# Optimization experiments

Measured on AMD Instinct MI355X. Metric: run time of the kernel, lower is better.

## Reference

```python
import jax, jax.numpy as jnp
import numpy as np

H1 = 51  # lstm1 hidden size
H2 = 1   # lstm2 hidden size


def _lstm_cell(x, h, c, Wih, Whh, bih, bhh):
    # PyTorch LSTMCell: gates = x W_ih^T + b_ih + h W_hh^T + b_hh, order i,f,g,o
    gates = x @ Wih.T + h @ Whh.T + (bih + bhh)
    i, f, g, o = jnp.split(gates, 4, axis=-1)
    i = jax.nn.sigmoid(i)
    f = jax.nn.sigmoid(f)
    g = jnp.tanh(g)
    o = jax.nn.sigmoid(o)
    c_new = f * c + i * g
    h_new = o * jnp.tanh(c_new)
    return h_new, c_new


def setup_inputs() -> dict:
    key = jax.random.key(0)
    ks = jax.random.split(key, 9)
    B, T = 2048, 1024
    s1 = 1.0 / np.sqrt(H1)
    s2 = 1.0 / np.sqrt(H2)
    u = lambda k, shape, s: jax.random.uniform(k, shape, jnp.float32, -s, s)
    return {
        "input": jax.random.normal(ks[0], (B, T), dtype=jnp.float32),
        "W_ih1": u(ks[1], (4 * H1, 1), s1),
        "W_hh1": u(ks[2], (4 * H1, H1), s1),
        "b_ih1": u(ks[3], (4 * H1,), s1),
        "b_hh1": u(ks[4], (4 * H1,), s1),
        "W_ih2": u(ks[5], (4 * H2, H1), s2),
        "W_hh2": u(ks[6], (4 * H2, H2), s2),
        "b_ih2": u(ks[7], (4 * H2,), s2),
        "b_hh2": u(ks[8], (4 * H2,), s2),
        "future": 64,
    }


def reference(input, W_ih1, W_hh1, b_ih1, b_hh1, W_ih2, W_hh2, b_ih2, b_hh2, future):
    B = input.shape[0]
    dt = input.dtype
    h1 = jnp.zeros((B, H1), dt)
    c1 = jnp.zeros((B, H1), dt)
    h2 = jnp.zeros((B, H2), dt)
    c2 = jnp.zeros((B, H2), dt)

    def step(carry, x_t):
        h1, c1, h2, c2 = carry
        h1, c1 = _lstm_cell(x_t, h1, c1, W_ih1, W_hh1, b_ih1, b_hh1)
        h2, c2 = _lstm_cell(h1, h2, c2, W_ih2, W_hh2, b_ih2, b_hh2)
        return (h1, c1, h2, c2), h2

    xs = jnp.swapaxes(input, 0, 1)[:, :, None]  # [T, B, 1]
    carry, outs = jax.lax.scan(step, (h1, c1, h2, c2), xs)

    def step_future(carry, _):
        h1, c1, h2, c2 = carry
        h1, c1 = _lstm_cell(h2, h1, c1, W_ih1, W_hh1, b_ih1, b_hh1)
        h2, c2 = _lstm_cell(h1, h2, c2, W_ih2, W_hh2, b_ih2, b_hh2)
        return (h1, c1, h2, c2), h2

    if future > 0:
        _, outs_f = jax.lax.scan(step_future, carry, None, length=future)
        outs = jnp.concatenate([outs, outs_f], axis=0)

    # [T+F, B, 1] -> [B, T+F]
    return jnp.swapaxes(outs[:, :, 0], 0, 1)
```

## Files before the change

kernel.cpp:

```cpp
#include <hip/hip_runtime.h>


#define H1N 51
#define NP  26
#define WAVE 64

typedef float v2f __attribute__((ext_vector_type(2)));

#define INV_LN2  1.44269504088896340736f
#define INV_LN2X2 2.88539008177792681472f

__device__ __forceinline__ float sigmoid_s(float xs) {
    return __builtin_amdgcn_rcpf(1.0f + __builtin_amdgcn_exp2f(-xs));
}
__device__ __forceinline__ float tanh_s2(float xs2) {
    float e = __builtin_amdgcn_exp2f(xs2);
    return fmaf(-2.0f, __builtin_amdgcn_rcpf(e + 1.0f), 1.0f);
}
__device__ __forceinline__ float tanh_nat(float x) {
    return tanh_s2(x * INV_LN2X2);
}
__device__ __forceinline__ float rdlane(float v, int k) {
    return __int_as_float(__builtin_amdgcn_readlane(__float_as_int(v), k));
}

template<int CTRL, int RM, int BM>
__device__ __forceinline__ void dpp_stage4(float& a, float& b, float& c, float& d) {
    int ta = __builtin_amdgcn_update_dpp(0, __float_as_int(a), CTRL, RM, BM, false);
    int tb = __builtin_amdgcn_update_dpp(0, __float_as_int(b), CTRL, RM, BM, false);
    int tc = __builtin_amdgcn_update_dpp(0, __float_as_int(c), CTRL, RM, BM, false);
    int td = __builtin_amdgcn_update_dpp(0, __float_as_int(d), CTRL, RM, BM, false);
    a += __int_as_float(ta); b += __int_as_float(tb);
    c += __int_as_float(tc); d += __int_as_float(td);
}

__global__ __attribute__((amdgpu_flat_work_group_size(64, 64),
                          amdgpu_waves_per_eu(2, 2)))
void lstm_seq(const float* __restrict__ input,
              const float* __restrict__ W_ih1,
              const float* __restrict__ W_hh1,
              const float* __restrict__ b_ih1,
              const float* __restrict__ b_hh1,
              const float* __restrict__ W_ih2,
              const float* __restrict__ W_hh2,
              const float* __restrict__ b_ih2,
              const float* __restrict__ b_hh2,
              float* __restrict__ out,
              int T, int TF)
{
    const int j   = threadIdx.x;
    const bool jv = (j < H1N);
    const int jj  = jv ? j : 0;
    const float m = jv ? 1.0f : 0.0f;
    const int b   = blockIdx.x;

    const int r_i = jj, r_f = H1N + jj, r_g = 2*H1N + jj, r_o = 3*H1N + jj;

    const float s_i = m * INV_LN2, s_f = m * INV_LN2;
    const float s_g = m * INV_LN2X2, s_o = m * INV_LN2;

    v2f wI[NP], wF[NP], wG[NP], wO[NP];
#pragma unroll
    for (int kk = 0; kk < NP; ++kk) {
        const int k0 = 2*kk, k1 = 2*kk + 1;
        const float n0 = (k0 < H1N) ? 1.0f : 0.0f;
        const float n1 = (k1 < H1N) ? 1.0f : 0.0f;
        const int c0 = (k0 < H1N) ? k0 : 0, c1i = (k1 < H1N) ? k1 : 0;
        wI[kk].x = s_i * n0 * W_hh1[r_i*H1N + c0];  wI[kk].y = s_i * n1 * W_hh1[r_i*H1N + c1i];
        wF[kk].x = s_f * n0 * W_hh1[r_f*H1N + c0];  wF[kk].y = s_f * n1 * W_hh1[r_f*H1N + c1i];
        wG[kk].x = s_g * n0 * W_hh1[r_g*H1N + c0];  wG[kk].y = s_g * n1 * W_hh1[r_g*H1N + c1i];
        wO[kk].x = s_o * n0 * W_hh1[r_o*H1N + c0];  wO[kk].y = s_o * n1 * W_hh1[r_o*H1N + c1i];
    }
    const float b_i = s_i * (b_ih1[r_i] + b_hh1[r_i]);
    const float b_f = s_f * (b_ih1[r_f] + b_hh1[r_f]);
    const float b_g = s_g * (b_ih1[r_g] + b_hh1[r_g]);
    const float b_o = s_o * (b_ih1[r_o] + b_hh1[r_o]);
    const float wx_i = s_i * W_ih1[r_i];
    const float wx_f = s_f * W_ih1[r_f];
    const float wx_g = s_g * W_ih1[r_g];
    const float wx_o = s_o * W_ih1[r_o];

    float wi2_0 = m * INV_LN2   * W_ih2[0*H1N + jj];
    float wi2_1 = m * INV_LN2   * W_ih2[1*H1N + jj];
    float wi2_2 = m * INV_LN2X2 * W_ih2[2*H1N + jj];
    float wi2_3 = m * INV_LN2   * W_ih2[3*H1N + jj];
    const float wh2_0 = INV_LN2*W_hh2[0], wh2_1 = INV_LN2*W_hh2[1];
    const float wh2_2 = INV_LN2X2*W_hh2[2], wh2_3 = INV_LN2*W_hh2[3];
    const float b2_0 = INV_LN2*(b_ih2[0] + b_hh2[0]), b2_1 = INV_LN2*(b_ih2[1] + b_hh2[1]);
    const float b2_2 = INV_LN2X2*(b_ih2[2] + b_hh2[2]), b2_3 = INV_LN2*(b_ih2[3] + b_hh2[3]);

    float h1 = 0.0f, c1 = 0.0f, h2 = 0.0f, c2 = 0.0f;

    const float* __restrict__ xrow = input + (long)b * T;
    float*       __restrict__ orow = out   + (long)b * TF;

    float xbuf = 0.0f;
    float obuf = 0.0f;

    for (int t = 0; t < TF; ++t) {
        asm volatile("" : "+v"(wi2_0), "+v"(wi2_1), "+v"(wi2_2), "+v"(wi2_3));

        float x;
        if (t < T) {
            if ((t & 63) == 0) xbuf = xrow[t + j];
            x = rdlane(xbuf, t & 63);
        } else {
            x = h2;
        }

        v2f aI = {fmaf(wx_i, x, b_i), 0.0f};
        v2f aF = {fmaf(wx_f, x, b_f), 0.0f};
        v2f aG = {fmaf(wx_g, x, b_g), 0.0f};
        v2f aO = {fmaf(wx_o, x, b_o), 0.0f};
#pragma unroll
        for (int kk = 0; kk < NP; ++kk) {
            const unsigned int hlo =
                (unsigned int)__builtin_amdgcn_readlane(__float_as_int(h1), 2*kk);
            const unsigned int hhi =
                (unsigned int)__builtin_amdgcn_readlane(__float_as_int(h1), 2*kk + 1);
            const unsigned long long hp =
                ((unsigned long long)hhi << 32) | (unsigned long long)hlo;
            asm("v_pk_fma_f32 %0, %4, %8, %0\n\t"
                "v_pk_fma_f32 %1, %5, %8, %1\n\t"
                "v_pk_fma_f32 %2, %6, %8, %2\n\t"
                "v_pk_fma_f32 %3, %7, %8, %3"
                : "+v"(aI), "+v"(aF), "+v"(aG), "+v"(aO),
                  "+v"(wI[kk]), "+v"(wF[kk]), "+v"(wG[kk]), "+v"(wO[kk])
                : "s"(hp));
        }
        const float gi = sigmoid_s(aI.x + aI.y);
        const float gf = sigmoid_s(aF.x + aF.y);
        const float gg = tanh_s2 (aG.x + aG.y);
        const float go = sigmoid_s(aO.x + aO.y);
        c1 = fmaf(gf, c1, gi * gg);
        h1 = go * tanh_nat(c1);

        float p0 = wi2_0 * h1, p1 = wi2_1 * h1, p2 = wi2_2 * h1, p3 = wi2_3 * h1;
        dpp_stage4<0x111, 0xf, 0xf>(p0, p1, p2, p3);
        dpp_stage4<0x112, 0xf, 0xf>(p0, p1, p2, p3);
        dpp_stage4<0x114, 0xf, 0xe>(p0, p1, p2, p3);
        dpp_stage4<0x118, 0xf, 0xc>(p0, p1, p2, p3);
        dpp_stage4<0x142, 0xa, 0xf>(p0, p1, p2, p3);
        dpp_stage4<0x143, 0xc, 0xf>(p0, p1, p2, p3);
        p0 = rdlane(p0, 63); p1 = rdlane(p1, 63);
        p2 = rdlane(p2, 63); p3 = rdlane(p3, 63);

        const float g2i = sigmoid_s(fmaf(wh2_0, h2, b2_0 + p0));
        const float g2f = sigmoid_s(fmaf(wh2_1, h2, b2_1 + p1));
        const float g2g = tanh_s2 (fmaf(wh2_2, h2, b2_2 + p2));
        const float g2o = sigmoid_s(fmaf(wh2_3, h2, b2_3 + p3));
        c2 = fmaf(g2f, c2, g2i * g2g);
        h2 = g2o * tanh_nat(c2);

        if (j == (t & 63)) obuf = h2;
        if ((t & 63) == 63) orow[t - 63 + j] = obuf;
    }
}

extern "C" void kernel_launch(void* const* d_in, const int* in_sizes, int n_in,
                              void* d_out, int out_size, void* d_ws, size_t ws_size,
                              hipStream_t stream) {
    const float* input = (const float*)d_in[0];
    const float* W_ih1 = (const float*)d_in[1];
    const float* W_hh1 = (const float*)d_in[2];
    const float* b_ih1 = (const float*)d_in[3];
    const float* b_hh1 = (const float*)d_in[4];
    const float* W_ih2 = (const float*)d_in[5];
    const float* W_hh2 = (const float*)d_in[6];
    const float* b_ih2 = (const float*)d_in[7];
    const float* b_hh2 = (const float*)d_in[8];
    float* out = (float*)d_out;

    const int B  = 2048;
    const int T  = in_sizes[0] / B;
    const int TF = out_size   / B;

    lstm_seq<<<dim3(B), dim3(WAVE), 0, stream>>>(
        input, W_ih1, W_hh1, b_ih1, b_hh1, W_ih2, W_hh2, b_ih2, b_hh2,
        out, T, TF);
}
```

Baseline: 1.321 ms.

## Split LSTM into layer-1 pass, batched layer-2 pass, and future pass

During the teacher-forced phase the layer-2 cell does not feed back into layer 1, so the single fused kernel is split in three. The first kernel runs the layer-1 recurrence and writes the four reduced layer-2 input projections per step to workspace. A second kernel, one thread per batch row, runs the scalar layer-2 recurrence, and a third handles the autoregressive future steps. Layer 1 now reads h1 from LDS instead of readlane broadcasts, which takes the serial layer-2 chain off the layer-1 critical path, at the cost of about 32MB of extra workspace traffic and two more launches.

New measurement: 1.505 ms. 1.14x slower.

```diff
diff --git a/kernel.cpp b/kernel.cpp
--- a/kernel.cpp
+++ b/kernel.cpp
@@ -4,10 +4,11 @@
 #define H1N 51
 #define NP  26
 #define WAVE 64
+#define BATCH 2048
 
 typedef float v2f __attribute__((ext_vector_type(2)));
 
-#define INV_LN2  1.44269504088896340736f
+#define INV_LN2   1.44269504088896340736f
 #define INV_LN2X2 2.88539008177792681472f
 
 __device__ __forceinline__ float sigmoid_s(float xs) {
@@ -33,20 +34,27 @@
     a += __int_as_float(ta); b += __int_as_float(tb);
     c += __int_as_float(tc); d += __int_as_float(td);
 }
+__device__ __forceinline__ void wave_sum4(float& p0, float& p1, float& p2, float& p3) {
+    dpp_stage4<0x111, 0xf, 0xf>(p0, p1, p2, p3);
+    dpp_stage4<0x112, 0xf, 0xf>(p0, p1, p2, p3);
+    dpp_stage4<0x114, 0xf, 0xe>(p0, p1, p2, p3);
+    dpp_stage4<0x118, 0xf, 0xc>(p0, p1, p2, p3);
+    dpp_stage4<0x142, 0xa, 0xf>(p0, p1, p2, p3);
+    dpp_stage4<0x143, 0xc, 0xf>(p0, p1, p2, p3);
+}
 
 __global__ __attribute__((amdgpu_flat_work_group_size(64, 64),
                           amdgpu_waves_per_eu(2, 2)))
-void lstm_seq(const float* __restrict__ input,
-              const float* __restrict__ W_ih1,
-              const float* __restrict__ W_hh1,
-              const float* __restrict__ b_ih1,
-              const float* __restrict__ b_hh1,
-              const float* __restrict__ W_ih2,
-              const float* __restrict__ W_hh2,
-              const float* __restrict__ b_ih2,
-              const float* __restrict__ b_hh2,
-              float* __restrict__ out,
-              int T, int TF)
+void lstm1_pass(const float* __restrict__ input,
+                const float* __restrict__ W_ih1,
+                const float* __restrict__ W_hh1,
+                const float* __restrict__ b_ih1,
+                const float* __restrict__ b_hh1,
+                const float* __restrict__ W_ih2,
+                float4* __restrict__ zws,
+                float* __restrict__ h1s,
+                float* __restrict__ c1s,
+                int T)
 {
     const int j   = threadIdx.x;
     const bool jv = (j < H1N);
@@ -55,7 +63,6 @@
     const int b   = blockIdx.x;
 
     const int r_i = jj, r_f = H1N + jj, r_g = 2*H1N + jj, r_o = 3*H1N + jj;
-
     const float s_i = m * INV_LN2, s_f = m * INV_LN2;
     const float s_g = m * INV_LN2X2, s_o = m * INV_LN2;
 
@@ -84,29 +91,142 @@
     float wi2_1 = m * INV_LN2   * W_ih2[1*H1N + jj];
     float wi2_2 = m * INV_LN2X2 * W_ih2[2*H1N + jj];
     float wi2_3 = m * INV_LN2   * W_ih2[3*H1N + jj];
+
+    __shared__ __align__(16) float hrow[64];
+    hrow[j] = 0.0f;
+
+    float h1 = 0.0f, c1 = 0.0f;
+    const float* __restrict__ xrow = input + (long)b * T;
+    float xbuf = 0.0f;
+
+    for (int t = 0; t < T; ++t) {
+        asm volatile("" : "+v"(wi2_0), "+v"(wi2_1), "+v"(wi2_2), "+v"(wi2_3));
+
+        if ((t & 63) == 0) xbuf = xrow[t + j];
+        const float x = rdlane(xbuf, t & 63);
+
+        v2f aI = {fmaf(wx_i, x, b_i), 0.0f};
+        v2f aF = {fmaf(wx_f, x, b_f), 0.0f};
+        v2f aG = {fmaf(wx_g, x, b_g), 0.0f};
+        v2f aO = {fmaf(wx_o, x, b_o), 0.0f};
+#pragma unroll
+        for (int kk = 0; kk < NP; ++kk) {
+            const v2f hp = *(const v2f*)&hrow[2*kk];
+            asm("v_pk_fma_f32 %0, %4, %8, %0\n\t"
+                "v_pk_fma_f32 %1, %5, %8, %1\n\t"
+                "v_pk_fma_f32 %2, %6, %8, %2\n\t"
+                "v_pk_fma_f32 %3, %7, %8, %3"
+                : "+v"(aI), "+v"(aF), "+v"(aG), "+v"(aO),
+                  "+v"(wI[kk]), "+v"(wF[kk]), "+v"(wG[kk]), "+v"(wO[kk])
+                : "v"(hp));
+        }
+        const float gi = sigmoid_s(aI.x + aI.y);
+        const float gf = sigmoid_s(aF.x + aF.y);
+        const float gg = tanh_s2 (aG.x + aG.y);
+        const float go = sigmoid_s(aO.x + aO.y);
+        c1 = fmaf(gf, c1, gi * gg);
+        h1 = go * tanh_nat(c1);
+
+        hrow[j] = jv ? h1 : 0.0f;
+
+        float p0 = wi2_0 * h1, p1 = wi2_1 * h1, p2 = wi2_2 * h1, p3 = wi2_3 * h1;
+        wave_sum4(p0, p1, p2, p3);
+        if (j == 63) zws[(long)t * BATCH + b] = make_float4(p0, p1, p2, p3);
+    }
+
+    if (jv) { h1s[b*H1N + j] = h1; c1s[b*H1N + j] = c1; }
+}
+
+__global__ void lstm2_pass(const float4* __restrict__ zws,
+                           const float* __restrict__ W_hh2,
+                           const float* __restrict__ b_ih2,
+                           const float* __restrict__ b_hh2,
+                           float* __restrict__ out,
+                           float2* __restrict__ h2c2,
+                           int T, int TF)
+{
+    const int s = blockIdx.x * WAVE + threadIdx.x;
     const float wh2_0 = INV_LN2*W_hh2[0], wh2_1 = INV_LN2*W_hh2[1];
     const float wh2_2 = INV_LN2X2*W_hh2[2], wh2_3 = INV_LN2*W_hh2[3];
     const float b2_0 = INV_LN2*(b_ih2[0] + b_hh2[0]), b2_1 = INV_LN2*(b_ih2[1] + b_hh2[1]);
     const float b2_2 = INV_LN2X2*(b_ih2[2] + b_hh2[2]), b2_3 = INV_LN2*(b_ih2[3] + b_hh2[3]);
 
-    float h1 = 0.0f, c1 = 0.0f, h2 = 0.0f, c2 = 0.0f;
-
-    const float* __restrict__ xrow = input + (long)b * T;
-    float*       __restrict__ orow = out   + (long)b * TF;
-
-    float xbuf = 0.0f;
+    float h2 = 0.0f, c2 = 0.0f;
+    float* __restrict__ orow = out + (long)s * TF;
+    for (int t = 0; t < T; ++t) {
+        const float4 z = zws[(long)t * BATCH + s];
+        const float g2i = sigmoid_s(fmaf(wh2_0, h2, b2_0 + z.x));
+        const float g2f = sigmoid_s(fmaf(wh2_1, h2, b2_1 + z.y));
+        const float g2g = tanh_s2 (fmaf(wh2_2, h2, b2_2 + z.z));
+        const float g2o = sigmoid_s(fmaf(wh2_3, h2, b2_3 + z.w));
+        c2 = fmaf(g2f, c2, g2i * g2g);
+        h2 = g2o * tanh_nat(c2);
+        orow[t] = h2;
+    }
+    h2c2[s] = make_float2(h2, c2);
+}
+
+__global__ __attribute__((amdgpu_flat_work_group_size(64, 64),
+                          amdgpu_waves_per_eu(2, 2)))
+void lstm_future(const float* __restrict__ W_ih1, const float* __restrict__ W_hh1,
+                 const float* __restrict__ b_ih1, const float* __restrict__ b_hh1,
+                 const float* __restrict__ W_ih2, const float* __restrict__ W_hh2,
+                 const float* __restrict__ b_ih2, const float* __restrict__ b_hh2,
+                 const float* __restrict__ h1s, const float* __restrict__ c1s,
+                 const float2* __restrict__ h2c2,
+                 float* __restrict__ out, int T, int TF)
+{
+    const int j   = threadIdx.x;
+    const bool jv = (j < H1N);
+    const int jj  = jv ? j : 0;
+    const float m = jv ? 1.0f : 0.0f;
+    const int b   = blockIdx.x;
+
+    const int r_i = jj, r_f = H1N + jj, r_g = 2*H1N + jj, r_o = 3*H1N + jj;
+    const float s_i = m * INV_LN2, s_f = m * INV_LN2;
+    const float s_g = m * INV_LN2X2, s_o = m * INV_LN2;
+
+    v2f wI[NP], wF[NP], wG[NP], wO[NP];
+#pragma unroll
+    for (int kk = 0; kk < NP; ++kk) {
+        const int k0 = 2*kk, k1 = 2*kk + 1;
+        const float n0 = (k0 < H1N) ? 1.0f : 0.0f;
+        const float n1 = (k1 < H1N) ? 1.0f : 0.0f;
+        const int c0 = (k0 < H1N) ? k0 : 0, c1i = (k1 < H1N) ? k1 : 0;
+        wI[kk].x = s_i * n0 * W_hh1[r_i*H1N + c0];  wI[kk].y = s_i * n1 * W_hh1[r_i*H1N + c1i];
+        wF[kk].x = s_f * n0 * W_hh1[r_f*H1N + c0];  wF[kk].y = s_f * n1 * W_hh1[r_f*H1N + c1i];
+        wG[kk].x = s_g * n0 * W_hh1[r_g*H1N + c0];  wG[kk].y = s_g * n1 * W_hh1[r_g*H1N + c1i];
+        wO[kk].x = s_o * n0 * W_hh1[r_o*H1N + c0];  wO[kk].y = s_o * n1 * W_hh1[r_o*H1N + c1i];
+    }
+    const float b_i = s_i * (b_ih1[r_i] + b_hh1[r_i]);
+    const float b_f = s_f * (b_ih1[r_f] + b_hh1[r_f]);
+    const float b_g = s_g * (b_ih1[r_g] + b_hh1[r_g]);
+    const float b_o = s_o * (b_ih1[r_o] + b_hh1[r_o]);
+    const float wx_i = s_i * W_ih1[r_i];
+    const float wx_f = s_f * W_ih1[r_f];
+    const float wx_g = s_g * W_ih1[r_g];
+    const float wx_o = s_o * W_ih1[r_o];
+
+    float wi2_0 = m * INV_LN2   * W_ih2[0*H1N + jj];
+    float wi2_1 = m * INV_LN2   * W_ih2[1*H1N + jj];
+    float wi2_2 = m * INV_LN2X2 * W_ih2[2*H1N + jj];
+    float wi2_3 = m * INV_LN2   * W_ih2[3*H1N + jj];
+    const float wh2_0 = INV_LN2*W_hh2[0], wh2_1 = INV_LN2*W_hh2[1];
+    const float wh2_2 = INV_LN2X2*W_hh2[2], wh2_3 = INV_LN2*W_hh2[3];
+    const float b2_0 = INV_LN2*(b_ih2[0] + b_hh2[0]), b2_1 = INV_LN2*(b_ih2[1] + b_hh2[1]);
+    const float b2_2 = INV_LN2X2*(b_ih2[2] + b_hh2[2]), b2_3 = INV_LN2*(b_ih2[3] + b_hh2[3]);
+
+    float h1 = jv ? h1s[b*H1N + jj] : 0.0f;
+    float c1 = jv ? c1s[b*H1N + jj] : 0.0f;
+    const float2 st = h2c2[b];
+    float h2 = st.x, c2 = st.y;
+
+    float* __restrict__ orow = out + (long)b * TF;
     float obuf = 0.0f;
 
-    for (int t = 0; t < TF; ++t) {
+    for (int t = T; t < TF; ++t) {
         asm volatile("" : "+v"(wi2_0), "+v"(wi2_1), "+v"(wi2_2), "+v"(wi2_3));
-
-        float x;
-        if (t < T) {
-            if ((t & 63) == 0) xbuf = xrow[t + j];
-            x = rdlane(xbuf, t & 63);
-        } else {
-            x = h2;
-        }
+        const float x = h2;
 
         v2f aI = {fmaf(wx_i, x, b_i), 0.0f};
         v2f aF = {fmaf(wx_f, x, b_f), 0.0f};
@@ -136,12 +256,7 @@
         h1 = go * tanh_nat(c1);
 
         float p0 = wi2_0 * h1, p1 = wi2_1 * h1, p2 = wi2_2 * h1, p3 = wi2_3 * h1;
-        dpp_stage4<0x111, 0xf, 0xf>(p0, p1, p2, p3);
-        dpp_stage4<0x112, 0xf, 0xf>(p0, p1, p2, p3);
-        dpp_stage4<0x114, 0xf, 0xe>(p0, p1, p2, p3);
-        dpp_stage4<0x118, 0xf, 0xc>(p0, p1, p2, p3);
-        dpp_stage4<0x142, 0xa, 0xf>(p0, p1, p2, p3);
-        dpp_stage4<0x143, 0xc, 0xf>(p0, p1, p2, p3);
+        wave_sum4(p0, p1, p2, p3);
         p0 = rdlane(p0, 63); p1 = rdlane(p1, 63);
         p2 = rdlane(p2, 63); p3 = rdlane(p3, 63);
 
@@ -171,11 +286,22 @@
     const float* b_hh2 = (const float*)d_in[8];
     float* out = (float*)d_out;
 
-    const int B  = 2048;
+    const int B  = BATCH;
     const int T  = in_sizes[0] / B;
     const int TF = out_size   / B;
 
-    lstm_seq<<<dim3(B), dim3(WAVE), 0, stream>>>(
-        input, W_ih1, W_hh1, b_ih1, b_hh1, W_ih2, W_hh2, b_ih2, b_hh2,
-        out, T, TF);
-}
+    char* ws = (char*)d_ws;
+    float4* zws = (float4*)ws;
+    size_t off = (size_t)T * B * sizeof(float4);
+    float* h1s = (float*)(ws + off);  off += (size_t)B * H1N * sizeof(float);
+    float* c1s = (float*)(ws + off);  off += (size_t)B * H1N * sizeof(float);
+    float2* h2c2 = (float2*)(ws + off);
+
+    lstm1_pass<<<dim3(B), dim3(WAVE), 0, stream>>>(
+        input, W_ih1, W_hh1, b_ih1, b_hh1, W_ih2, zws, h1s, c1s, T);
+    lstm2_pass<<<dim3(B / WAVE), dim3(WAVE), 0, stream>>>(
+        zws, W_hh2, b_ih2, b_hh2, out, h2c2, T, TF);
+    lstm_future<<<dim3(B), dim3(WAVE), 0, stream>>>(
+        W_ih1, W_hh1, b_ih1, b_hh1, W_ih2, W_hh2, b_ih2, b_hh2,
+        h1s, c1s, h2c2, out, T, TF);
+}
```

## Process two sequences per wave and fold layer-2 projection into layer-1 matvec

Applied to the files above, without the earlier changes.

Each wave now handles two batch rows, sharing the register-resident W_hh1 weights across both recurrent matvecs. The hidden state is broadcast through LDS vector loads instead of per-element readlanes. The layer-2 input projection is folded into spare lanes 51-54 of the layer-1 matvec, with the bias packed into the padding column, which removes the DPP reduction. Layer 2 is skewed by one step, and occupancy drops to one wave per EU. The aim is less per-step latency per sequence, in exchange for fewer waves, more registers, and LDS round trips with no explicit barriers inside a single-wave block.

After: 1.290 ms. 2.3% less time.

```diff
diff --git a/kernel.cpp b/kernel.cpp
--- a/kernel.cpp
+++ b/kernel.cpp
@@ -1,13 +1,13 @@
 #include <hip/hip_runtime.h>
 
 
-#define H1N 51
-#define NP  26
+#define H1N  51
+#define NP   26
 #define WAVE 64
 
 typedef float v2f __attribute__((ext_vector_type(2)));
 
-#define INV_LN2  1.44269504088896340736f
+#define INV_LN2   1.44269504088896340736f
 #define INV_LN2X2 2.88539008177792681472f
 
 __device__ __forceinline__ float sigmoid_s(float xs) {
@@ -24,136 +24,162 @@
     return __int_as_float(__builtin_amdgcn_readlane(__float_as_int(v), k));
 }
 
-template<int CTRL, int RM, int BM>
-__device__ __forceinline__ void dpp_stage4(float& a, float& b, float& c, float& d) {
-    int ta = __builtin_amdgcn_update_dpp(0, __float_as_int(a), CTRL, RM, BM, false);
-    int tb = __builtin_amdgcn_update_dpp(0, __float_as_int(b), CTRL, RM, BM, false);
-    int tc = __builtin_amdgcn_update_dpp(0, __float_as_int(c), CTRL, RM, BM, false);
-    int td = __builtin_amdgcn_update_dpp(0, __float_as_int(d), CTRL, RM, BM, false);
-    a += __int_as_float(ta); b += __int_as_float(tb);
-    c += __int_as_float(tc); d += __int_as_float(td);
-}
-
 __global__ __attribute__((amdgpu_flat_work_group_size(64, 64),
-                          amdgpu_waves_per_eu(2, 2)))
-void lstm_seq(const float* __restrict__ input,
-              const float* __restrict__ W_ih1,
-              const float* __restrict__ W_hh1,
-              const float* __restrict__ b_ih1,
-              const float* __restrict__ b_hh1,
-              const float* __restrict__ W_ih2,
-              const float* __restrict__ W_hh2,
-              const float* __restrict__ b_ih2,
-              const float* __restrict__ b_hh2,
-              float* __restrict__ out,
-              int T, int TF)
+                          amdgpu_waves_per_eu(1, 1)))
+void lstm_seq2(const float* __restrict__ input,
+               const float* __restrict__ W_ih1,
+               const float* __restrict__ W_hh1,
+               const float* __restrict__ b_ih1,
+               const float* __restrict__ b_hh1,
+               const float* __restrict__ W_ih2,
+               const float* __restrict__ W_hh2,
+               const float* __restrict__ b_ih2,
+               const float* __restrict__ b_hh2,
+               float* __restrict__ out,
+               int T, int TF)
 {
     const int j   = threadIdx.x;
     const bool jv = (j < H1N);
     const int jj  = jv ? j : 0;
     const float m = jv ? 1.0f : 0.0f;
-    const int b   = blockIdx.x;
+    const bool isz = (j >= H1N) && (j < H1N + 4);
+    const int  q   = isz ? (j - H1N) : 0;
+    const float mz = isz ? 1.0f : 0.0f;
+    const float s2q = (q == 2) ? INV_LN2X2 : INV_LN2;
+
+    const int sA = 2 * blockIdx.x, sB = sA + 1;
 
     const int r_i = jj, r_f = H1N + jj, r_g = 2*H1N + jj, r_o = 3*H1N + jj;
-
-    const float s_i = m * INV_LN2, s_f = m * INV_LN2;
-    const float s_g = m * INV_LN2X2, s_o = m * INV_LN2;
+    const float s_i = INV_LN2, s_f = INV_LN2, s_g = INV_LN2X2, s_o = INV_LN2;
 
     v2f wI[NP], wF[NP], wG[NP], wO[NP];
 #pragma unroll
     for (int kk = 0; kk < NP; ++kk) {
-        const int k0 = 2*kk, k1 = 2*kk + 1;
-        const float n0 = (k0 < H1N) ? 1.0f : 0.0f;
-        const float n1 = (k1 < H1N) ? 1.0f : 0.0f;
-        const int c0 = (k0 < H1N) ? k0 : 0, c1i = (k1 < H1N) ? k1 : 0;
-        wI[kk].x = s_i * n0 * W_hh1[r_i*H1N + c0];  wI[kk].y = s_i * n1 * W_hh1[r_i*H1N + c1i];
-        wF[kk].x = s_f * n0 * W_hh1[r_f*H1N + c0];  wF[kk].y = s_f * n1 * W_hh1[r_f*H1N + c1i];
-        wG[kk].x = s_g * n0 * W_hh1[r_g*H1N + c0];  wG[kk].y = s_g * n1 * W_hh1[r_g*H1N + c1i];
-        wO[kk].x = s_o * n0 * W_hh1[r_o*H1N + c0];  wO[kk].y = s_o * n1 * W_hh1[r_o*H1N + c1i];
+        const int k0 = 2*kk, k1 = k0 + 1;
+        wI[kk].x = m*s_i*W_hh1[r_i*H1N + k0] + mz*s2q*W_ih2[q*H1N + k0];
+        wF[kk].x = m*s_f*W_hh1[r_f*H1N + k0];
+        wG[kk].x = m*s_g*W_hh1[r_g*H1N + k0];
+        wO[kk].x = m*s_o*W_hh1[r_o*H1N + k0];
+        if (k1 < H1N) {
+            wI[kk].y = m*s_i*W_hh1[r_i*H1N + k1] + mz*s2q*W_ih2[q*H1N + k1];
+            wF[kk].y = m*s_f*W_hh1[r_f*H1N + k1];
+            wG[kk].y = m*s_g*W_hh1[r_g*H1N + k1];
+            wO[kk].y = m*s_o*W_hh1[r_o*H1N + k1];
+        } else {
+            wI[kk].y = m*s_i*(b_ih1[r_i] + b_hh1[r_i]);
+            wF[kk].y = m*s_f*(b_ih1[r_f] + b_hh1[r_f]);
+            wG[kk].y = m*s_g*(b_ih1[r_g] + b_hh1[r_g]);
+            wO[kk].y = m*s_o*(b_ih1[r_o] + b_hh1[r_o]);
+        }
     }
-    const float b_i = s_i * (b_ih1[r_i] + b_hh1[r_i]);
-    const float b_f = s_f * (b_ih1[r_f] + b_hh1[r_f]);
-    const float b_g = s_g * (b_ih1[r_g] + b_hh1[r_g]);
-    const float b_o = s_o * (b_ih1[r_o] + b_hh1[r_o]);
-    const float wx_i = s_i * W_ih1[r_i];
-    const float wx_f = s_f * W_ih1[r_f];
-    const float wx_g = s_g * W_ih1[r_g];
-    const float wx_o = s_o * W_ih1[r_o];
-
-    float wi2_0 = m * INV_LN2   * W_ih2[0*H1N + jj];
-    float wi2_1 = m * INV_LN2   * W_ih2[1*H1N + jj];
-    float wi2_2 = m * INV_LN2X2 * W_ih2[2*H1N + jj];
-    float wi2_3 = m * INV_LN2   * W_ih2[3*H1N + jj];
+    const float wx_i = m*s_i*W_ih1[r_i];
+    const float wx_f = m*s_f*W_ih1[r_f];
+    const float wx_g = m*s_g*W_ih1[r_g];
+    const float wx_o = m*s_o*W_ih1[r_o];
+
     const float wh2_0 = INV_LN2*W_hh2[0], wh2_1 = INV_LN2*W_hh2[1];
     const float wh2_2 = INV_LN2X2*W_hh2[2], wh2_3 = INV_LN2*W_hh2[3];
     const float b2_0 = INV_LN2*(b_ih2[0] + b_hh2[0]), b2_1 = INV_LN2*(b_ih2[1] + b_hh2[1]);
     const float b2_2 = INV_LN2X2*(b_ih2[2] + b_hh2[2]), b2_3 = INV_LN2*(b_ih2[3] + b_hh2[3]);
 
-    float h1 = 0.0f, c1 = 0.0f, h2 = 0.0f, c2 = 0.0f;
-
-    const float* __restrict__ xrow = input + (long)b * T;
-    float*       __restrict__ orow = out   + (long)b * TF;
-
-    float xbuf = 0.0f;
-    float obuf = 0.0f;
-
-    for (int t = 0; t < TF; ++t) {
-        asm volatile("" : "+v"(wi2_0), "+v"(wi2_1), "+v"(wi2_2), "+v"(wi2_3));
-
-        float x;
-        if (t < T) {
-            if ((t & 63) == 0) xbuf = xrow[t + j];
-            x = rdlane(xbuf, t & 63);
-        } else {
-            x = h2;
-        }
-
-        v2f aI = {fmaf(wx_i, x, b_i), 0.0f};
-        v2f aF = {fmaf(wx_f, x, b_f), 0.0f};
-        v2f aG = {fmaf(wx_g, x, b_g), 0.0f};
-        v2f aO = {fmaf(wx_o, x, b_o), 0.0f};
+    __shared__ __align__(16) float hrowA[WAVE];
+    __shared__ __align__(16) float hrowB[WAVE];
+    __shared__ __align__(16) float2 zbuf[4];
+    hrowA[j] = (j == H1N) ? 1.0f : 0.0f;
+    hrowB[j] = (j == H1N) ? 1.0f : 0.0f;
+
+    float h1A = 0.0f, c1A = 0.0f, h2A = 0.0f, c2A = 0.0f;
+    float h1B = 0.0f, c1B = 0.0f, h2B = 0.0f, c2B = 0.0f;
+
+    const float* __restrict__ xrowA = input + (long)sA * T;
+    const float* __restrict__ xrowB = input + (long)sB * T;
+    float* __restrict__ orowA = out + (long)sA * TF;
+    float* __restrict__ orowB = out + (long)sB * TF;
+
+    float xbufA = 0.0f, xbufB = 0.0f, obufA = 0.0f, obufB = 0.0f;
+
+    for (int n = 0; n <= TF; ++n) {
+        v2f aIA = {0.0f, 0.0f}, aFA = {0.0f, 0.0f};
+        v2f aGA = {0.0f, 0.0f}, aOA = {0.0f, 0.0f};
+        v2f aIB = {0.0f, 0.0f}, aFB = {0.0f, 0.0f};
+        v2f aGB = {0.0f, 0.0f}, aOB = {0.0f, 0.0f};
 #pragma unroll
         for (int kk = 0; kk < NP; ++kk) {
-            const unsigned int hlo =
-                (unsigned int)__builtin_amdgcn_readlane(__float_as_int(h1), 2*kk);
-            const unsigned int hhi =
-                (unsigned int)__builtin_amdgcn_readlane(__float_as_int(h1), 2*kk + 1);
-            const unsigned long long hp =
-                ((unsigned long long)hhi << 32) | (unsigned long long)hlo;
-            asm("v_pk_fma_f32 %0, %4, %8, %0\n\t"
-                "v_pk_fma_f32 %1, %5, %8, %1\n\t"
-                "v_pk_fma_f32 %2, %6, %8, %2\n\t"
-                "v_pk_fma_f32 %3, %7, %8, %3"
-                : "+v"(aI), "+v"(aF), "+v"(aG), "+v"(aO),
+            const v2f hpA = *(const v2f*)&hrowA[2*kk];
+            const v2f hpB = *(const v2f*)&hrowB[2*kk];
+            asm("v_pk_fma_f32 %0, %8,  %12, %0\n\t"
+                "v_pk_fma_f32 %4, %8,  %13, %4\n\t"
+                "v_pk_fma_f32 %1, %9,  %12, %1\n\t"
+                "v_pk_fma_f32 %5, %9,  %13, %5\n\t"
+                "v_pk_fma_f32 %2, %10, %12, %2\n\t"
+                "v_pk_fma_f32 %6, %10, %13, %6\n\t"
+                "v_pk_fma_f32 %3, %11, %12, %3\n\t"
+                "v_pk_fma_f32 %7, %11, %13, %7"
+                : "+v"(aIA), "+v"(aFA), "+v"(aGA), "+v"(aOA),
+                  "+v"(aIB), "+v"(aFB), "+v"(aGB), "+v"(aOB),
                   "+v"(wI[kk]), "+v"(wF[kk]), "+v"(wG[kk]), "+v"(wO[kk])
-                : "s"(hp));
-        }
-        const float gi = sigmoid_s(aI.x + aI.y);
-        const float gf = sigmoid_s(aF.x + aF.y);
-        const float gg = tanh_s2 (aG.x + aG.y);
-        const float go = sigmoid_s(aO.x + aO.y);
-        c1 = fmaf(gf, c1, gi * gg);
-        h1 = go * tanh_nat(c1);
-
-        float p0 = wi2_0 * h1, p1 = wi2_1 * h1, p2 = wi2_2 * h1, p3 = wi2_3 * h1;
-        dpp_stage4<0x111, 0xf, 0xf>(p0, p1, p2, p3);
-        dpp_stage4<0x112, 0xf, 0xf>(p0, p1, p2, p3);
-        dpp_stage4<0x114, 0xf, 0xe>(p0, p1, p2, p3);
-        dpp_stage4<0x118, 0xf, 0xc>(p0, p1, p2, p3);
-        dpp_stage4<0x142, 0xa, 0xf>(p0, p1, p2, p3);
-        dpp_stage4<0x143, 0xc, 0xf>(p0, p1, p2, p3);
-        p0 = rdlane(p0, 63); p1 = rdlane(p1, 63);
-        p2 = rdlane(p2, 63); p3 = rdlane(p3, 63);
-
-        const float g2i = sigmoid_s(fmaf(wh2_0, h2, b2_0 + p0));
-        const float g2f = sigmoid_s(fmaf(wh2_1, h2, b2_1 + p1));
-        const float g2g = tanh_s2 (fmaf(wh2_2, h2, b2_2 + p2));
-        const float g2o = sigmoid_s(fmaf(wh2_3, h2, b2_3 + p3));
-        c2 = fmaf(g2f, c2, g2i * g2g);
-        h2 = g2o * tanh_nat(c2);
-
-        if (j == (t & 63)) obuf = h2;
-        if ((t & 63) == 63) orow[t - 63 + j] = obuf;
+                : "v"(hpA), "v"(hpB));
+        }
+        const float mIA = aIA.x + aIA.y, mIB = aIB.x + aIB.y;
+        if (isz) zbuf[q] = make_float2(mIA, mIB);
+        const float mFA = aFA.x + aFA.y, mFB = aFB.x + aFB.y;
+        const float mGA = aGA.x + aGA.y, mGB = aGB.x + aGB.y;
+        const float mOA = aOA.x + aOA.y, mOB = aOB.x + aOB.y;
+
+        if (n > 0) {
+            const float2 z0 = zbuf[0], z1 = zbuf[1], z2 = zbuf[2], z3 = zbuf[3];
+            {
+                const float g2i = sigmoid_s(fmaf(wh2_0, h2A, b2_0 + z0.x));
+                const float g2f = sigmoid_s(fmaf(wh2_1, h2A, b2_1 + z1.x));
+                const float g2g = tanh_s2 (fmaf(wh2_2, h2A, b2_2 + z2.x));
+                const float g2o = sigmoid_s(fmaf(wh2_3, h2A, b2_3 + z3.x));
+                c2A = fmaf(g2f, c2A, g2i * g2g);
+                h2A = g2o * tanh_nat(c2A);
+            }
+            {
+                const float g2i = sigmoid_s(fmaf(wh2_0, h2B, b2_0 + z0.y));
+                const float g2f = sigmoid_s(fmaf(wh2_1, h2B, b2_1 + z1.y));
+                const float g2g = tanh_s2 (fmaf(wh2_2, h2B, b2_2 + z2.y));
+                const float g2o = sigmoid_s(fmaf(wh2_3, h2B, b2_3 + z3.y));
+                c2B = fmaf(g2f, c2B, g2i * g2g);
+                h2B = g2o * tanh_nat(c2B);
+            }
+            const int tt = n - 1;
+            if (j == (tt & 63)) { obufA = h2A; obufB = h2B; }
+            if ((tt & 63) == 63) {
+                orowA[tt - 63 + j] = obufA;
+                orowB[tt - 63 + j] = obufB;
+            }
+        }
+
+        if (n < TF) {
+            float xA, xB;
+            if (n < T) {
+                if ((n & 63) == 0) { xbufA = xrowA[n + j]; xbufB = xrowB[n + j]; }
+                xA = rdlane(xbufA, n & 63);
+                xB = rdlane(xbufB, n & 63);
+            } else {
+                xA = h2A;
+                xB = h2B;
+            }
+            {
+                const float gi = sigmoid_s(fmaf(wx_i, xA, mIA));
+                const float gf = sigmoid_s(fmaf(wx_f, xA, mFA));
+                const float gg = tanh_s2 (fmaf(wx_g, xA, mGA));
+                const float go = sigmoid_s(fmaf(wx_o, xA, mOA));
+                c1A = fmaf(gf, c1A, gi * gg);
+                h1A = go * tanh_nat(c1A);
+            }
+            {
+                const float gi = sigmoid_s(fmaf(wx_i, xB, mIB));
+                const float gf = sigmoid_s(fmaf(wx_f, xB, mFB));
+                const float gg = tanh_s2 (fmaf(wx_g, xB, mGB));
+                const float go = sigmoid_s(fmaf(wx_o, xB, mOB));
+                c1B = fmaf(gf, c1B, gi * gg);
+                h1B = go * tanh_nat(c1B);
+            }
+            if (jv) { hrowA[j] = h1A; hrowB[j] = h1B; }
+        }
     }
 }
 
@@ -175,7 +201,7 @@
     const int T  = in_sizes[0] / B;
     const int TF = out_size   / B;
 
-    lstm_seq<<<dim3(B), dim3(WAVE), 0, stream>>>(
+    lstm_seq2<<<dim3(B / 2), dim3(WAVE), 0, stream>>>(
         input, W_ih1, W_hh1, b_ih1, b_hh1, W_ih2, W_hh2, b_ih2, b_hh2,
         out, T, TF);
 }
```
